# Optimization experiments

Measured on AMD Instinct MI355X. Metric: run time of the kernel, lower is better.

Reference implementation:

```python
import jax, jax.numpy as jnp
import numpy as np

D_MODEL = 2048
NUM_HEADS = 32
NUM_KV_GROUPS = 8
D_K = D_MODEL // NUM_HEADS  # 64
KV_DIM = D_K * NUM_KV_GROUPS  # 512
B, S = 2, 2048


def setup_inputs() -> dict:
    key = jax.random.key(0)
    ks = jax.random.split(key, 9)
    sd = 1.0 / np.sqrt(D_MODEL).astype(np.float32)
    return {
        "x": jax.random.normal(ks[0], (B, S, D_MODEL), jnp.float32),
        "wq": jax.random.normal(ks[1], (D_MODEL, D_MODEL), jnp.float32) * sd,
        "bq": jnp.zeros((D_MODEL,), jnp.float32),
        "wk": jax.random.normal(ks[2], (D_MODEL, KV_DIM), jnp.float32) * sd,
        "bk": jnp.zeros((KV_DIM,), jnp.float32),
        "wv": jax.random.normal(ks[3], (D_MODEL, KV_DIM), jnp.float32) * sd,
        "bv": jnp.zeros((KV_DIM,), jnp.float32),
        "wo": jax.random.normal(ks[4], (D_MODEL, D_MODEL), jnp.float32) * sd,
        "bo": jnp.zeros((D_MODEL,), jnp.float32),
    }


def reference(x, wq, bq, wk, bk, wv, bv, wo, bo):
    b, s, _ = x.shape
    # projections (torch Linear = x @ W^T + b; weights here stored as (in,out))
    Q = (x @ wq + bq).reshape(b, s, NUM_HEADS, D_K).transpose(0, 2, 1, 3)       # [B,H,S,dk]
    K = (x @ wk + bk).reshape(b, s, NUM_KV_GROUPS, D_K).transpose(0, 2, 1, 3)   # [B,G,S,dk]
    V = (x @ wv + bv).reshape(b, s, NUM_KV_GROUPS, D_K).transpose(0, 2, 1, 3)   # [B,G,S,dk]
    kv_repeat = NUM_HEADS // NUM_KV_GROUPS
    K_rep = jnp.repeat(K, kv_repeat, axis=1)  # [B,H,S,dk]
    V_rep = jnp.repeat(V, kv_repeat, axis=1)  # [B,H,S,dk]
    scale = 1.0 / jnp.sqrt(jnp.asarray(D_K, x.dtype))
    attn_scores = jnp.einsum("bhqd,bhkd->bhqk", Q, K_rep) * scale
    attn_weights = jax.nn.softmax(attn_scores, axis=-1)                          # [B,H,S,S]
    context = jnp.einsum("bhqk,bhkd->bhqd", attn_weights, V_rep)
    context = context.transpose(0, 2, 1, 3).reshape(b, s, D_MODEL)
    return context @ wo + bo
```

## Files before the change

kernel.cpp:

```cpp
#include <hip/hip_runtime.h>
#include <hip/hip_bf16.h>

typedef __bf16 v8bf16 __attribute__((ext_vector_type(8)));
typedef __bf16 bf16x4 __attribute__((ext_vector_type(4)));
typedef float  f32x4  __attribute__((ext_vector_type(4)));

#define D_MODEL 2048
#define S_LEN   2048
#define NHEADS  32
#define NGROUPS 8
#define DK      64
#define NTOK    4096
#define NQKV    3072
#define QSCALE  0.18033688011112042f

__device__ __forceinline__ void lds_load16(const void* g, void* l) {
  __builtin_amdgcn_global_load_lds(
      (__attribute__((address_space(1))) unsigned int*)g,
      (__attribute__((address_space(3))) unsigned int*)l, 16, 0, 0);
}

__global__ __launch_bounds__(256)
void cvt_f32_bf16(const float* __restrict__ in, __bf16* __restrict__ out, int n) {
  int i = (blockIdx.x * 256 + threadIdx.x) * 4;
  if (i >= n) return;
  float4 v = *(const float4*)(in + i);
  bf16x4 o = { (__bf16)v.x, (__bf16)v.y, (__bf16)v.z, (__bf16)v.w };
  *(bf16x4*)(out + i) = o;
}

__global__ __launch_bounds__(256)
void transpose_cvt(const float* __restrict__ in, __bf16* __restrict__ out, int R, int C) {
  __shared__ float tile[32][33];
  int tx = threadIdx.x, ty = threadIdx.y;
  int c0 = blockIdx.x * 32, r0 = blockIdx.y * 32;
#pragma unroll
  for (int j = 0; j < 4; j++)
    tile[ty + 8 * j][tx] = in[(size_t)(r0 + ty + 8 * j) * C + c0 + tx];
  __syncthreads();
#pragma unroll
  for (int j = 0; j < 4; j++)
    out[(size_t)(c0 + ty + 8 * j) * R + r0 + tx] = (__bf16)tile[tx][ty + 8 * j];
}

__global__ __launch_bounds__(256)
void transpose_bf16(const __bf16* __restrict__ in, __bf16* __restrict__ out,
                    int R, int C, int ldin, int ldout) {
  __shared__ __bf16 tile[32][33];
  int tx = threadIdx.x, ty = threadIdx.y;
  int c0 = blockIdx.x * 32, r0 = blockIdx.y * 32;
#pragma unroll
  for (int j = 0; j < 4; j++)
    tile[ty + 8 * j][tx] = in[(size_t)(r0 + ty + 8 * j) * ldin + c0 + tx];
  __syncthreads();
#pragma unroll
  for (int j = 0; j < 4; j++)
    out[(size_t)(c0 + ty + 8 * j) * ldout + r0 + tx] = tile[tx][ty + 8 * j];
}

template <int MODE>
__global__ __launch_bounds__(256, 2)
void gemm_bt(const __bf16* __restrict__ A, const __bf16* __restrict__ BT,
             const float* __restrict__ b0, const float* __restrict__ b1,
             const float* __restrict__ b2,
             __bf16* __restrict__ Cb, float* __restrict__ Cf,
             int M, int N, int K) {
  __shared__ __bf16 As[128 * 32];
  __shared__ __bf16 Bs[128 * 32];
  const int t = threadIdx.x;
  const int lane = t & 63, w = t >> 6;
  const int lr = lane & 15, lg = lane >> 4;
  const int gx = gridDim.x;
  const int flat = blockIdx.y * gx + blockIdx.x;
  const int cpx = (gx * gridDim.y) >> 3;
  const int sb = (flat & 7) * cpx + (flat >> 3);
  const int m0 = (sb / gx) * 128, n0 = (sb % gx) * 128;
  const int rm = (w >> 1) * 64, cn = (w & 1) * 64;
  const int srow = t >> 2, scol = (t & 3) * 8;

  const f32x4 fz = {0.f, 0.f, 0.f, 0.f};
  f32x4 acc[4][4];
#pragma unroll
  for (int mi = 0; mi < 4; mi++)
#pragma unroll
    for (int ni = 0; ni < 4; ni++) acc[mi][ni] = fz;

  for (int kt = 0; kt < K; kt += 32) {
    __syncthreads();
    lds_load16(A + (size_t)(m0 + srow) * K + kt + scol, As + w * 512);
    lds_load16(A + (size_t)(m0 + 64 + srow) * K + kt + scol, As + 2048 + w * 512);
    lds_load16(BT + (size_t)(n0 + srow) * K + kt + scol, Bs + w * 512);
    lds_load16(BT + (size_t)(n0 + 64 + srow) * K + kt + scol, Bs + 2048 + w * 512);
    __syncthreads();
    v8bf16 af[4], bfr[4];
#pragma unroll
    for (int i = 0; i < 4; i++)
      af[i] = *(const v8bf16*)&As[(rm + i * 16 + lr) * 32 + lg * 8];
#pragma unroll
    for (int i = 0; i < 4; i++)
      bfr[i] = *(const v8bf16*)&Bs[(cn + i * 16 + lr) * 32 + lg * 8];
#pragma unroll
    for (int mi = 0; mi < 4; mi++)
#pragma unroll
      for (int ni = 0; ni < 4; ni++)
        acc[mi][ni] = __builtin_amdgcn_mfma_f32_16x16x32_bf16(af[mi], bfr[ni], acc[mi][ni], 0, 0, 0);
  }

#pragma unroll
  for (int ni = 0; ni < 4; ni++) {
    int col = n0 + cn + ni * 16 + lr;
    float bias, scale = 1.0f;
    if (MODE == 0) {
      if (col < 2048)      { bias = b0[col];        scale = QSCALE; }
      else if (col < 2560) { bias = b1[col - 2048]; }
      else                 { bias = b2[col - 2560]; }
    } else {
      bias = b0[col];
    }
#pragma unroll
    for (int mi = 0; mi < 4; mi++)
#pragma unroll
      for (int r = 0; r < 4; r++) {
        int row = m0 + rm + mi * 16 + lg * 4 + r;
        float v = acc[mi][ni][r] + bias;
        if (MODE == 0) Cb[(size_t)row * N + col] = (__bf16)(v * scale);
        else           Cf[(size_t)row * N + col] = v;
      }
  }
}

__global__ __launch_bounds__(512, 2)
void attn_kernel(const __bf16* __restrict__ QKV, const __bf16* __restrict__ VT,
                 __bf16* __restrict__ ctx) {
  __shared__ __bf16 smem[34816];
  const int t = threadIdx.x;
  const int lane = t & 63, w = t >> 6;
  const int lr = lane & 15, lg = lane >> 4;
  const int flat = blockIdx.y * 8 + blockIdx.x;
  const int swz = (flat & 7) * 64 + (flat >> 3);
  const int qt = swz & 7, bh = swz >> 3;
  const int b = bh >> 5, h = bh & 31, g = h >> 2;
  const int q0 = qt * 256;
  const int scol = (((t & 7) ^ ((t >> 3) & 7)) << 3);

  v8bf16 qa[2][2];
#pragma unroll
  for (int mi = 0; mi < 2; mi++)
#pragma unroll
    for (int dk2 = 0; dk2 < 2; dk2++)
      qa[mi][dk2] = *(const v8bf16*)(QKV +
          (size_t)(b * S_LEN + q0 + w * 32 + mi * 16 + lr) * NQKV + h * DK + dk2 * 32 + lg * 8);

  const __bf16* kp = QKV + (size_t)(b * S_LEN + (t >> 3)) * NQKV + D_MODEL + g * DK + scol;
  const __bf16* vp = VT + (size_t)(g * DK + (t >> 3)) * NTOK + b * S_LEN + scol;

  auto stage = [&](__bf16* buf) {
    lds_load16(kp, buf + t * 8);
    lds_load16(vp, buf + 4096 + t * 8);
    kp += (size_t)64 * NQKV;
    vp += 64;
  };

  __bf16* bufA = smem;
  __bf16* bufB = smem + 8192;
  __bf16* bufC = smem + 16384;

  stage(bufA);
  stage(bufB);

  const int kloff0 = lr * 64 + ((lg * 8) ^ ((lr & 7) << 3));
  const int kloff1 = lr * 64 + ((32 + lg * 8) ^ ((lr & 7) << 3));
  __bf16* Pw = smem + 24576 + w * 1280;

  const __bf16 one1 = (__bf16)1.0f;
  const v8bf16 ones = { one1, one1, one1, one1, one1, one1, one1, one1 };
  const f32x4 fz = {0.f, 0.f, 0.f, 0.f};
  f32x4 o[2][4], o_sum[2];
  o_sum[0] = fz; o_sum[1] = fz;
#pragma unroll
  for (int mi = 0; mi < 2; mi++)
#pragma unroll
    for (int nd = 0; nd < 4; nd++) o[mi][nd] = fz;

  auto compute = [&](const __bf16* Kb) {
    const __bf16* k0 = Kb + kloff0;
    const __bf16* k1 = Kb + kloff1;
    f32x4 st[4][2];
#pragma unroll
    for (int ni = 0; ni < 4; ni++) { st[ni][0] = fz; st[ni][1] = fz; }
    __builtin_amdgcn_s_setprio(1);
#pragma unroll
    for (int ni = 0; ni < 4; ni++) {
      v8bf16 kb = *(const v8bf16*)(k0 + ni * 1024);
      st[ni][0] = __builtin_amdgcn_mfma_f32_16x16x32_bf16(kb, qa[0][0], st[ni][0], 0, 0, 0);
      st[ni][1] = __builtin_amdgcn_mfma_f32_16x16x32_bf16(kb, qa[1][0], st[ni][1], 0, 0, 0);
    }
#pragma unroll
    for (int ni = 0; ni < 4; ni++) {
      v8bf16 kb = *(const v8bf16*)(k1 + ni * 1024);
      st[ni][0] = __builtin_amdgcn_mfma_f32_16x16x32_bf16(kb, qa[0][1], st[ni][0], 0, 0, 0);
      st[ni][1] = __builtin_amdgcn_mfma_f32_16x16x32_bf16(kb, qa[1][1], st[ni][1], 0, 0, 0);
    }
    __builtin_amdgcn_s_setprio(0);

#pragma unroll
    for (int ks = 0; ks < 2; ks++) {
      const __bf16* vbase = (ks ? k1 : k0) + 4096;
#pragma unroll
      for (int mi = 0; mi < 2; mi++)
#pragma unroll
        for (int ni2 = 0; ni2 < 2; ni2++) {
          f32x4 sv = st[2 * ks + ni2][mi];
          bf16x4 pk = { (__bf16)exp2f(sv[0]), (__bf16)exp2f(sv[1]),
                        (__bf16)exp2f(sv[2]), (__bf16)exp2f(sv[3]) };
          *(bf16x4*)(Pw + (mi * 16 + lr) * 40 + ni2 * 16 + lg * 4) = pk;
        }
      v8bf16 pa0 = *(const v8bf16*)(Pw + lr * 40 + lg * 8);
      v8bf16 pa1 = *(const v8bf16*)(Pw + (16 + lr) * 40 + lg * 8);
      __builtin_amdgcn_s_setprio(1);
#pragma unroll
      for (int nd = 0; nd < 4; nd++) {
        v8bf16 vb = *(const v8bf16*)(vbase + nd * 1024);
        o[0][nd] = __builtin_amdgcn_mfma_f32_16x16x32_bf16(pa0, vb, o[0][nd], 0, 0, 0);
        o[1][nd] = __builtin_amdgcn_mfma_f32_16x16x32_bf16(pa1, vb, o[1][nd], 0, 0, 0);
      }
      o_sum[0] = __builtin_amdgcn_mfma_f32_16x16x32_bf16(pa0, ones, o_sum[0], 0, 0, 0);
      o_sum[1] = __builtin_amdgcn_mfma_f32_16x16x32_bf16(pa1, ones, o_sum[1], 0, 0, 0);
      __builtin_amdgcn_s_setprio(0);
    }
  };

  __bf16* cur = bufA;
  __bf16* nxt = bufB;
  __bf16* fre = bufC;
  for (int kt = 0; kt < 31; kt++) {
    asm volatile("s_waitcnt vmcnt(2)" ::: "memory");
    __builtin_amdgcn_s_barrier();
    __builtin_amdgcn_sched_barrier(0);
    if (kt < 30) stage(fre);
    compute(cur);
    __bf16* tmp = cur; cur = nxt; nxt = fre; fre = tmp;
  }
  asm volatile("s_waitcnt vmcnt(0)" ::: "memory");
  __builtin_amdgcn_s_barrier();
  __builtin_amdgcn_sched_barrier(0);
  compute(cur);

#pragma unroll
  for (int mi = 0; mi < 2; mi++)
#pragma unroll
    for (int r = 0; r < 4; r++) {
      float inv = 1.0f / o_sum[mi][r];
      int row = b * S_LEN + q0 + w * 32 + mi * 16 + lg * 4 + r;
#pragma unroll
      for (int nd = 0; nd < 4; nd++)
        ctx[(size_t)row * D_MODEL + h * DK + nd * 16 + lr] = (__bf16)(o[mi][nd][r] * inv);
    }
}

extern "C" void kernel_launch(void* const* d_in, const int* in_sizes, int n_in,
                              void* d_out, int out_size, void* d_ws, size_t ws_size,
                              hipStream_t stream) {
  (void)in_sizes; (void)n_in; (void)out_size; (void)ws_size;
  const float* x  = (const float*)d_in[0];
  const float* wq = (const float*)d_in[1];
  const float* bq = (const float*)d_in[2];
  const float* wk = (const float*)d_in[3];
  const float* bk = (const float*)d_in[4];
  const float* wv = (const float*)d_in[5];
  const float* bv = (const float*)d_in[6];
  const float* wo = (const float*)d_in[7];
  const float* bo = (const float*)d_in[8];

  char* ws = (char*)d_ws;
  __bf16* xb    = (__bf16*)(ws);
  __bf16* wqkvT = (__bf16*)(ws + 16777216);
  __bf16* woT   = (__bf16*)(ws + 29360128);
  __bf16* QKVb  = (__bf16*)(ws + 37748736);
  __bf16* VbT   = (__bf16*)(ws + 62914560);
  __bf16* ctx   = (__bf16*)(ws + 67108864);

  dim3 tb(32, 8);
  cvt_f32_bf16<<<8192, 256, 0, stream>>>(x, xb, NTOK * D_MODEL);
  transpose_cvt<<<dim3(64, 64), tb, 0, stream>>>(wq, wqkvT, 2048, 2048);
  transpose_cvt<<<dim3(16, 64), tb, 0, stream>>>(wk, wqkvT + 2048 * 2048, 2048, 512);
  transpose_cvt<<<dim3(16, 64), tb, 0, stream>>>(wv, wqkvT + 2560 * 2048, 2048, 512);
  transpose_cvt<<<dim3(64, 64), tb, 0, stream>>>(wo, woT, 2048, 2048);

  gemm_bt<0><<<dim3(24, 32), 256, 0, stream>>>(xb, wqkvT, bq, bk, bv,
                                               QKVb, nullptr, NTOK, NQKV, 2048);
  transpose_bf16<<<dim3(16, 128), tb, 0, stream>>>(QKVb + 2560, VbT, 4096, 512, 3072, 4096);
  attn_kernel<<<dim3(8, 64), 512, 0, stream>>>(QKVb, VbT, ctx);
  gemm_bt<1><<<dim3(16, 32), 256, 0, stream>>>(ctx, woT, bo, nullptr, nullptr,
                                               nullptr, (float*)d_out, NTOK, 2048, 2048);
}
```

Baseline: 229.9 us.

## Switch attention kernel to 32x32x16 MFMA tiles

Rewrites the attention inner loop to use 32x32x16 bf16 MFMA instructions in place of 16x16x32, which changes the Q register layout, the K/V LDS read pattern, the P staging layout and the output write mapping. Larger MFMA tiles cut the instruction count and the LDS reads per FLOP. In exchange each wave needs larger accumulator registers and its LDS access pattern changes, and both could affect bank conflicts or occupancy.

```diff
diff --git a/kernel.cpp b/kernel.cpp
--- a/kernel.cpp
+++ b/kernel.cpp
@@ -4,6 +4,7 @@
 typedef __bf16 v8bf16 __attribute__((ext_vector_type(8)));
 typedef __bf16 bf16x4 __attribute__((ext_vector_type(4)));
 typedef float  f32x4  __attribute__((ext_vector_type(4)));
+typedef float  f32x16 __attribute__((ext_vector_type(16)));
 
 #define D_MODEL 2048
 #define S_LEN   2048
@@ -135,7 +136,7 @@
   __shared__ __bf16 smem[34816];
   const int t = threadIdx.x;
   const int lane = t & 63, w = t >> 6;
-  const int lr = lane & 15, lg = lane >> 4;
+  const int lc = lane & 31, hi = lane >> 5;
   const int flat = blockIdx.y * 8 + blockIdx.x;
   const int swz = (flat & 7) * 64 + (flat >> 3);
   const int qt = swz & 7, bh = swz >> 3;
@@ -143,13 +144,11 @@
   const int q0 = qt * 256;
   const int scol = (((t & 7) ^ ((t >> 3) & 7)) << 3);
 
-  v8bf16 qa[2][2];
-#pragma unroll
-  for (int mi = 0; mi < 2; mi++)
-#pragma unroll
-    for (int dk2 = 0; dk2 < 2; dk2++)
-      qa[mi][dk2] = *(const v8bf16*)(QKV +
-          (size_t)(b * S_LEN + q0 + w * 32 + mi * 16 + lr) * NQKV + h * DK + dk2 * 32 + lg * 8);
+  v8bf16 qb[4];
+#pragma unroll
+  for (int m = 0; m < 4; m++)
+    qb[m] = *(const v8bf16*)(QKV +
+        (size_t)(b * S_LEN + q0 + w * 32 + lc) * NQKV + h * DK + m * 16 + hi * 8);
 
   const __bf16* kp = QKV + (size_t)(b * S_LEN + (t >> 3)) * NQKV + D_MODEL + g * DK + scol;
   const __bf16* vp = VT + (size_t)(g * DK + (t >> 3)) * NTOK + b * S_LEN + scol;
@@ -168,64 +167,56 @@
   stage(bufA);
   stage(bufB);
 
-  const int kloff0 = lr * 64 + ((lg * 8) ^ ((lr & 7) << 3));
-  const int kloff1 = lr * 64 + ((32 + lg * 8) ^ ((lr & 7) << 3));
+  int coloff[4];
+#pragma unroll
+  for (int m = 0; m < 4; m++)
+    coloff[m] = (m * 16 + hi * 8) ^ ((lc & 7) << 3);
+
   __bf16* Pw = smem + 24576 + w * 1280;
+  __bf16* ppw = Pw + lc * 40 + hi * 4;
+  const __bf16* ppr = Pw + lc * 40 + hi * 8;
 
   const __bf16 one1 = (__bf16)1.0f;
   const v8bf16 ones = { one1, one1, one1, one1, one1, one1, one1, one1 };
-  const f32x4 fz = {0.f, 0.f, 0.f, 0.f};
-  f32x4 o[2][4], o_sum[2];
-  o_sum[0] = fz; o_sum[1] = fz;
-#pragma unroll
-  for (int mi = 0; mi < 2; mi++)
-#pragma unroll
-    for (int nd = 0; nd < 4; nd++) o[mi][nd] = fz;
+  const f32x16 fz16 = {0.f,0.f,0.f,0.f,0.f,0.f,0.f,0.f,0.f,0.f,0.f,0.f,0.f,0.f,0.f,0.f};
+  f32x16 o[2], osum;
+  o[0] = fz16; o[1] = fz16; osum = fz16;
 
   auto compute = [&](const __bf16* Kb) {
-    const __bf16* k0 = Kb + kloff0;
-    const __bf16* k1 = Kb + kloff1;
-    f32x4 st[4][2];
-#pragma unroll
-    for (int ni = 0; ni < 4; ni++) { st[ni][0] = fz; st[ni][1] = fz; }
+    const __bf16* kb0 = Kb + lc * 64;
+    const __bf16* vb0 = Kb + 4096 + lc * 64;
+    f32x16 st[2];
+    st[0] = fz16; st[1] = fz16;
     __builtin_amdgcn_s_setprio(1);
 #pragma unroll
-    for (int ni = 0; ni < 4; ni++) {
-      v8bf16 kb = *(const v8bf16*)(k0 + ni * 1024);
-      st[ni][0] = __builtin_amdgcn_mfma_f32_16x16x32_bf16(kb, qa[0][0], st[ni][0], 0, 0, 0);
-      st[ni][1] = __builtin_amdgcn_mfma_f32_16x16x32_bf16(kb, qa[1][0], st[ni][1], 0, 0, 0);
-    }
-#pragma unroll
-    for (int ni = 0; ni < 4; ni++) {
-      v8bf16 kb = *(const v8bf16*)(k1 + ni * 1024);
-      st[ni][0] = __builtin_amdgcn_mfma_f32_16x16x32_bf16(kb, qa[0][1], st[ni][0], 0, 0, 0);
-      st[ni][1] = __builtin_amdgcn_mfma_f32_16x16x32_bf16(kb, qa[1][1], st[ni][1], 0, 0, 0);
+    for (int m = 0; m < 4; m++) {
+      v8bf16 ka0 = *(const v8bf16*)(kb0 + coloff[m]);
+      v8bf16 ka1 = *(const v8bf16*)(kb0 + 2048 + coloff[m]);
+      st[0] = __builtin_amdgcn_mfma_f32_32x32x16_bf16(ka0, qb[m], st[0], 0, 0, 0);
+      st[1] = __builtin_amdgcn_mfma_f32_32x32x16_bf16(ka1, qb[m], st[1], 0, 0, 0);
     }
     __builtin_amdgcn_s_setprio(0);
 
 #pragma unroll
-    for (int ks = 0; ks < 2; ks++) {
-      const __bf16* vbase = (ks ? k1 : k0) + 4096;
-#pragma unroll
-      for (int mi = 0; mi < 2; mi++)
-#pragma unroll
-        for (int ni2 = 0; ni2 < 2; ni2++) {
-          f32x4 sv = st[2 * ks + ni2][mi];
-          bf16x4 pk = { (__bf16)exp2f(sv[0]), (__bf16)exp2f(sv[1]),
-                        (__bf16)exp2f(sv[2]), (__bf16)exp2f(sv[3]) };
-          *(bf16x4*)(Pw + (mi * 16 + lr) * 40 + ni2 * 16 + lg * 4) = pk;
-        }
-      v8bf16 pa0 = *(const v8bf16*)(Pw + lr * 40 + lg * 8);
-      v8bf16 pa1 = *(const v8bf16*)(Pw + (16 + lr) * 40 + lg * 8);
+    for (int t2 = 0; t2 < 2; t2++) {
+#pragma unroll
+      for (int u = 0; u < 4; u++) {
+        bf16x4 pk = { (__bf16)exp2f(st[t2][4 * u + 0]), (__bf16)exp2f(st[t2][4 * u + 1]),
+                      (__bf16)exp2f(st[t2][4 * u + 2]), (__bf16)exp2f(st[t2][4 * u + 3]) };
+        *(bf16x4*)(ppw + u * 8) = pk;
+      }
+      v8bf16 pa0 = *(const v8bf16*)(ppr);
+      v8bf16 pa1 = *(const v8bf16*)(ppr + 16);
       __builtin_amdgcn_s_setprio(1);
 #pragma unroll
-      for (int nd = 0; nd < 4; nd++) {
-        v8bf16 vb = *(const v8bf16*)(vbase + nd * 1024);
-        o[0][nd] = __builtin_amdgcn_mfma_f32_16x16x32_bf16(pa0, vb, o[0][nd], 0, 0, 0);
-        o[1][nd] = __builtin_amdgcn_mfma_f32_16x16x32_bf16(pa1, vb, o[1][nd], 0, 0, 0);
+      for (int k4 = 0; k4 < 2; k4++) {
+        v8bf16 pa = k4 ? pa1 : pa0;
+        v8bf16 vq0 = *(const v8bf16*)(vb0 + coloff[t2 * 2 + k4]);
+        v8bf16 vq1 = *(const v8bf16*)(vb0 + 2048 + coloff[t2 * 2 + k4]);
+        o[0] = __builtin_amdgcn_mfma_f32_32x32x16_bf16(pa, vq0, o[0], 0, 0, 0);
+        o[1] = __builtin_amdgcn_mfma_f32_32x32x16_bf16(pa, vq1, o[1], 0, 0, 0);
+        osum = __builtin_amdgcn_mfma_f32_32x32x16_bf16(pa, ones, osum, 0, 0, 0);
       }
-      o_sum[0] = __builtin_amdgcn_mfma_f32_16x16x32_bf16(pa0, ones, o_sum[0], 0, 0, 0);
-      o_sum[1] = __builtin_amdgcn_mfma_f32_16x16x32_bf16(pa1, ones, o_sum[1], 0, 0, 0);
       __builtin_amdgcn_s_setprio(0);
     }
   };
@@ -247,15 +238,12 @@
   compute(cur);
 
 #pragma unroll
-  for (int mi = 0; mi < 2; mi++)
-#pragma unroll
-    for (int r = 0; r < 4; r++) {
-      float inv = 1.0f / o_sum[mi][r];
-      int row = b * S_LEN + q0 + w * 32 + mi * 16 + lg * 4 + r;
-#pragma unroll
-      for (int nd = 0; nd < 4; nd++)
-        ctx[(size_t)row * D_MODEL + h * DK + nd * 16 + lr] = (__bf16)(o[mi][nd][r] * inv);
-    }
+  for (int r = 0; r < 16; r++) {
+    float inv = 1.0f / osum[r];
+    int row = b * S_LEN + q0 + w * 32 + (r & 3) + 8 * (r >> 2) + 4 * hi;
+    ctx[(size_t)row * D_MODEL + h * DK + lc]      = (__bf16)(o[0][r] * inv);
+    ctx[(size_t)row * D_MODEL + h * DK + 32 + lc] = (__bf16)(o[1][r] * inv);
+  }
 }
 
 extern "C" void kernel_launch(void* const* d_in, const int* in_sizes, int n_in,
```

Result: slower. 251.7 us (+9.5%).
